# Optimization experiments

Hardware: AMD Instinct MI355X
Metric: run time of the kernel (lower is better)

Reference implementation:

```python
import jax, jax.numpy as jnp
import numpy as np

DIM = 1024
HEADS = 16
HEAD_DIM = 64
INNER = HEADS * HEAD_DIM  # 1024
SCALE = 8.0
LN_EPS = 1e-5
NORM_EPS = 1e-12  # F.normalize default eps


def layer_norm(x, g, b):
    m = jnp.mean(x, axis=-1, keepdims=True)
    v = jnp.mean((x - m) ** 2, axis=-1, keepdims=True)
    return (x - m) * jax.lax.rsqrt(v + LN_EPS) * g + b


def l2_normalize(x):
    n = jnp.sqrt(jnp.sum(x * x, axis=-1, keepdims=True))
    return x / jnp.maximum(n, NORM_EPS)


def setup_inputs() -> dict:
    key = jax.random.key(0)
    ks = jax.random.split(key, 8)
    B, N, T = 4, 4096, 256
    s = 0.02
    return {
        "x": jax.random.normal(ks[0], (B, N, DIM), jnp.float32),
        "context": jax.random.normal(ks[1], (B, T, DIM), jnp.float32),
        "Wq": jax.random.normal(ks[2], (DIM, INNER), jnp.float32) * s,
        "Wkv": jax.random.normal(ks[3], (DIM, 2 * INNER), jnp.float32) * s,
        "Wo": jax.random.normal(ks[4], (INNER, DIM), jnp.float32) * s,
        "null_kv": jax.random.normal(ks[5], (2, HEAD_DIM), jnp.float32),
        "q_scale": jnp.ones((HEAD_DIM,), jnp.float32),
        "k_scale": jnp.ones((HEAD_DIM,), jnp.float32),
        "ln_in_g": jnp.ones((DIM,), jnp.float32),
        "ln_in_b": jnp.zeros((DIM,), jnp.float32),
        "ln_ctx_g": jnp.ones((DIM,), jnp.float32),
        "ln_ctx_b": jnp.zeros((DIM,), jnp.float32),
        "ln_out_g": jnp.ones((DIM,), jnp.float32),
        "ln_out_b": jnp.zeros((DIM,), jnp.float32),
    }


def reference(x, context, Wq, Wkv, Wo, null_kv, q_scale, k_scale,
              ln_in_g, ln_in_b, ln_ctx_g, ln_ctx_b, ln_out_g, ln_out_b):
    B, N, _ = x.shape
    T = context.shape[1]
    xn = layer_norm(x, ln_in_g, ln_in_b)
    cn = layer_norm(context, ln_ctx_g, ln_ctx_b)
    q = xn @ Wq                      # [B, N, INNER]
    kv = cn @ Wkv                    # [B, T, 2*INNER]
    k, v = jnp.split(kv, 2, axis=-1)
    # split heads: b s (h d) -> b h s d
    def split_heads(t):
        b, s, _ = t.shape
        return t.reshape(b, s, HEADS, HEAD_DIM).transpose(0, 2, 1, 3)
    q, k, v = split_heads(q), split_heads(k), split_heads(v)
    # null kv token appended along kv-seq dim
    nk = jnp.broadcast_to(null_kv[0], (B, HEADS, 1, HEAD_DIM))
    nv = jnp.broadcast_to(null_kv[1], (B, HEADS, 1, HEAD_DIM))
    k = jnp.concatenate([k, nk], axis=2)   # [B, H, T+1, D]
    v = jnp.concatenate([v, nv], axis=2)
    q = l2_normalize(q) * q_scale
    k = l2_normalize(k) * k_scale
    scores = jnp.einsum('bhid,bhkd->bhik', q, k) * SCALE
    attn = jax.nn.softmax(scores, axis=-1)
    out = jnp.einsum('bhik,bhkd->bhid', attn, v)   # [B, H, N, D]
    out = out.transpose(0, 2, 1, 3).reshape(B, N, INNER)
    out = out @ Wo
    return layer_norm(out, ln_out_g, ln_out_b)
```

## Files before the change

### kernel.cpp

```cpp
#include <hip/hip_runtime.h>
#include <cstdint>
#include <cstddef>

typedef _Float16 f16;
typedef _Float16 f16x4 __attribute__((ext_vector_type(4)));
typedef _Float16 f16x8 __attribute__((ext_vector_type(8)));
typedef float f32x4 __attribute__((ext_vector_type(4)));

#define DIM 1024
#define B_ 4
#define N_ 4096
#define TKP 288
#define SCALE_ 8.0f
#define LOG2E 1.4426950408889634f

__device__ __forceinline__ void gload_lds16(const void* g, void* l) {
  __builtin_amdgcn_global_load_lds(
      reinterpret_cast<const __attribute__((address_space(1))) uint32_t*>(
          reinterpret_cast<uintptr_t>(g)),
      reinterpret_cast<__attribute__((address_space(3))) uint32_t*>(
          reinterpret_cast<uintptr_t>(l)),
      16, 0, 0);
}

__global__ void transpose_w_kernel(const float* __restrict__ W, f16* __restrict__ WT,
                                   int K, int N) {
  __shared__ float tile[32][33];
  int nt = N >> 5;
  int tk = blockIdx.x / nt, tn = blockIdx.x % nt;
  int tx = threadIdx.x & 31, ty = threadIdx.x >> 5;
#pragma unroll
  for (int p = 0; p < 32; p += 8)
    tile[ty + p][tx] = W[(size_t)(tk * 32 + ty + p) * N + tn * 32 + tx];
  __syncthreads();
#pragma unroll
  for (int p = 0; p < 32; p += 8)
    WT[(size_t)(tn * 32 + ty + p) * K + tk * 32 + tx] = (f16)tile[tx][ty + p];
}

template <typename OUT_T>
__global__ void ln_kernel(const float* __restrict__ in, const float* __restrict__ g,
                          const float* __restrict__ bb, OUT_T* __restrict__ out) {
  int row = blockIdx.x;
  int t = threadIdx.x;
  const float4* rp = (const float4*)(in + (size_t)row * DIM);
  float4 v = rp[t];
  float s = v.x + v.y + v.z + v.w;
  float ss = v.x * v.x + v.y * v.y + v.z * v.z + v.w * v.w;
#pragma unroll
  for (int m = 1; m < 64; m <<= 1) { s += __shfl_xor(s, m); ss += __shfl_xor(ss, m); }
  __shared__ float red[8];
  int w = t >> 6;
  if ((t & 63) == 0) { red[w * 2] = s; red[w * 2 + 1] = ss; }
  __syncthreads();
  s = red[0] + red[2] + red[4] + red[6];
  ss = red[1] + red[3] + red[5] + red[7];
  float mean = s * (1.0f / DIM);
  float var = ss * (1.0f / DIM) - mean * mean;
  float rstd = rsqrtf(var + 1e-5f);
  float4 gv = ((const float4*)g)[t];
  float4 bv = ((const float4*)bb)[t];
  float o0 = (v.x - mean) * rstd * gv.x + bv.x;
  float o1 = (v.y - mean) * rstd * gv.y + bv.y;
  float o2 = (v.z - mean) * rstd * gv.z + bv.z;
  float o3 = (v.w - mean) * rstd * gv.w + bv.w;
  if constexpr (sizeof(OUT_T) == 2) {
    f16x4 h = {(f16)o0, (f16)o1, (f16)o2, (f16)o3};
    *(f16x4*)((f16*)out + (size_t)row * DIM + t * 4) = h;
  } else {
    float4 o = {o0, o1, o2, o3};
    *(float4*)((float*)out + (size_t)row * DIM + t * 4) = o;
  }
}

template <bool OUT_F32>
__global__ __launch_bounds__(256, 2) void gemm_nt_kernel(
    const f16* __restrict__ A, const f16* __restrict__ Bt, void* __restrict__ C,
    int M, int N, int K) {
  __shared__ f16 As[128 * 64];
  __shared__ f16 Bs[128 * 64];
  int nb = N >> 7;
  int cpx = gridDim.x >> 3;
  int wg = ((int)blockIdx.x & 7) * cpx + ((int)blockIdx.x >> 3);
  int bm = wg / nb, bn = wg % nb;
  int t = threadIdx.x;
  int lane = t & 63, w = t >> 6;
  int wm = w >> 1, wn = w & 1;
  int r16 = lane & 15, g4 = lane >> 4;
  f32x4 acc[4][4] = {};
  for (int k0 = 0; k0 < K; k0 += 64) {
#pragma unroll
    for (int i = 0; i < 4; ++i) {
      int li = i * 256 + t;
      int r = li >> 3, c = li & 7;
      int kc = ((c ^ (r & 7)) << 3);
      gload_lds16(A + (size_t)(bm * 128 + r) * K + k0 + kc, (char*)As + li * 16);
      gload_lds16(Bt + (size_t)(bn * 128 + r) * K + k0 + kc, (char*)Bs + li * 16);
    }
    asm volatile("s_waitcnt vmcnt(0)" ::: "memory");
    __syncthreads();
#pragma unroll
    for (int ks = 0; ks < 2; ++ks) {
      f16x8 af[4], bf[4];
#pragma unroll
      for (int mi = 0; mi < 4; ++mi) {
        int r = wm * 64 + mi * 16 + r16;
        int cidx = ks * 4 + g4;
        af[mi] = *(const f16x8*)(As + r * 64 + ((cidx ^ (r & 7)) << 3));
      }
#pragma unroll
      for (int ni = 0; ni < 4; ++ni) {
        int r = wn * 64 + ni * 16 + r16;
        int cidx = ks * 4 + g4;
        bf[ni] = *(const f16x8*)(Bs + r * 64 + ((cidx ^ (r & 7)) << 3));
      }
#pragma unroll
      for (int mi = 0; mi < 4; ++mi)
#pragma unroll
        for (int ni = 0; ni < 4; ++ni)
          acc[mi][ni] = __builtin_amdgcn_mfma_f32_16x16x32_f16(af[mi], bf[ni],
                                                               acc[mi][ni], 0, 0, 0);
    }
    __syncthreads();
  }
  int cr0 = bm * 128 + wm * 64;
  int cc = bn * 128 + wn * 64 + r16;
#pragma unroll
  for (int mi = 0; mi < 4; ++mi)
#pragma unroll
    for (int ni = 0; ni < 4; ++ni)
#pragma unroll
      for (int j = 0; j < 4; ++j) {
        int row = cr0 + mi * 16 + g4 * 4 + j;
        int col = cc + ni * 16;
        if constexpr (OUT_F32)
          ((float*)C)[(size_t)row * N + col] = acc[mi][ni][j];
        else
          ((f16*)C)[(size_t)row * N + col] = (f16)acc[mi][ni][j];
      }
}

__global__ void prep_kv_kernel(const f16* __restrict__ kv, const float* __restrict__ nullkv,
                               const float* __restrict__ ks, f16* __restrict__ Karr,
                               f16* __restrict__ Varr) {
  int bh = blockIdx.x;
  int b = bh >> 4, h = bh & 15;
  int t = threadIdx.x;
  __shared__ f16 vt[256][65];
  const f16* krow = kv + (size_t)(b * 256 + t) * 2048 + h * 64;
  const f16* vrow = krow + 1024;
  f16x8 kd[8];
  float ss = 0.0f;
#pragma unroll
  for (int i = 0; i < 8; ++i) {
    kd[i] = *(const f16x8*)(krow + i * 8);
#pragma unroll
    for (int j = 0; j < 8; ++j) { float x = (float)kd[i][j]; ss += x * x; }
  }
  float inv = 1.0f / fmaxf(sqrtf(ss), 1e-12f);
  f16* kout = Karr + ((size_t)bh * TKP + t) * 64;
#pragma unroll
  for (int i = 0; i < 8; ++i) {
    f16x8 o;
#pragma unroll
    for (int j = 0; j < 8; ++j) o[j] = (f16)((float)kd[i][j] * inv * ks[i * 8 + j]);
    *(f16x8*)(kout + i * 8) = o;
  }
#pragma unroll
  for (int i = 0; i < 8; ++i) {
    f16x8 vv = *(const f16x8*)(vrow + i * 8);
#pragma unroll
    for (int j = 0; j < 8; ++j) vt[t][i * 8 + j] = vv[j];
  }
  if (t < 32) {
    f16* kr = Karr + ((size_t)bh * TKP + 256 + t) * 64;
    if (t == 0) {
      float ssn = 0.0f;
      for (int d = 0; d < 64; ++d) ssn += nullkv[d] * nullkv[d];
      float invn = 1.0f / fmaxf(sqrtf(ssn), 1e-12f);
      for (int d = 0; d < 64; ++d) kr[d] = (f16)(nullkv[d] * invn * ks[d]);
    } else {
      for (int d = 0; d < 64; ++d) kr[d] = (f16)0.0f;
    }
  }
  __syncthreads();
  f16* vbase = Varr + (size_t)bh * 64 * TKP;
  for (int d = 0; d < 64; ++d) vbase[(size_t)d * TKP + t] = vt[t][d];
#pragma unroll
  for (int i = 0; i < 8; ++i) {
    int idx = i * 256 + t;
    int d = idx >> 5, key = 256 + (idx & 31);
    vbase[(size_t)d * TKP + key] = (key == 256) ? (f16)nullkv[64 + d] : (f16)0.0f;
  }
}

__global__ __launch_bounds__(256, 2) void attn_kernel(
    const f16* __restrict__ Q, const f16* __restrict__ Karr,
    const f16* __restrict__ Varr, const float* __restrict__ qs,
    f16* __restrict__ O) {
  int qb = blockIdx.x & 15, bh = blockIdx.x >> 4;
  int b = bh >> 4, h = bh & 15;
  int t = threadIdx.x, lane = t & 63, w = t >> 6;
  int r16 = lane & 15, g4 = lane >> 4;
  int row0 = b * N_ + qb * 256 + w * 64;
  int col0 = h * 64;
  const f16* Kp = Karr + (size_t)bh * TKP * 64;
  const f16* Vp = Varr + (size_t)bh * 64 * TKP;
  __shared__ f16 Plds[4][64 * 40];
  f16* Pw = &Plds[w][0];
  float qsv[2][8];
#pragma unroll
  for (int kdh = 0; kdh < 2; ++kdh)
#pragma unroll
    for (int i = 0; i < 8; ++i) qsv[kdh][i] = qs[kdh * 32 + g4 * 8 + i];
  f16x8 qf[4][2];
#pragma unroll
  for (int mi = 0; mi < 4; ++mi) {
    float f[2][8];
    float ssq = 0.0f;
#pragma unroll
    for (int kdh = 0; kdh < 2; ++kdh) {
      f16x8 v = *(const f16x8*)(Q + (size_t)(row0 + mi * 16 + r16) * DIM +
                                col0 + kdh * 32 + g4 * 8);
#pragma unroll
      for (int i = 0; i < 8; ++i) { f[kdh][i] = (float)v[i]; ssq += f[kdh][i] * f[kdh][i]; }
    }
    ssq += __shfl_xor(ssq, 16);
    ssq += __shfl_xor(ssq, 32);
    float inv = 1.0f / fmaxf(sqrtf(ssq), 1e-12f);
#pragma unroll
    for (int kdh = 0; kdh < 2; ++kdh) {
      f16x8 o;
#pragma unroll
      for (int i = 0; i < 8; ++i) o[i] = (f16)(f[kdh][i] * inv * qsv[kdh][i]);
      qf[mi][kdh] = o;
    }
  }
  f32x4 o[4][4] = {};
  float mrow[4][4], lrow[4][4];
#pragma unroll
  for (int mi = 0; mi < 4; ++mi)
#pragma unroll
    for (int j = 0; j < 4; ++j) { mrow[mi][j] = -1e30f; lrow[mi][j] = 0.0f; }
  for (int kt = 0; kt < 9; ++kt) {
    int key0 = kt * 32;
    f16x8 kf[2][2];
#pragma unroll
    for (int ni = 0; ni < 2; ++ni)
#pragma unroll
      for (int kdh = 0; kdh < 2; ++kdh)
        kf[ni][kdh] = *(const f16x8*)(Kp + (size_t)(key0 + ni * 16 + r16) * 64 +
                                      kdh * 32 + g4 * 8);
    f32x4 s[4][2] = {};
#pragma unroll
    for (int kdh = 0; kdh < 2; ++kdh)
#pragma unroll
      for (int mi = 0; mi < 4; ++mi)
#pragma unroll
        for (int ni = 0; ni < 2; ++ni)
          s[mi][ni] = __builtin_amdgcn_mfma_f32_16x16x32_f16(qf[mi][kdh], kf[ni][kdh],
                                                             s[mi][ni], 0, 0, 0);
    bool va = (key0 + r16 <= 256), vb = (key0 + 16 + r16 <= 256);
#pragma unroll
    for (int mi = 0; mi < 4; ++mi) {
#pragma unroll
      for (int j = 0; j < 4; ++j) {
        float s0 = va ? s[mi][0][j] * SCALE_ : -1e30f;
        float s1 = vb ? s[mi][1][j] * SCALE_ : -1e30f;
        float tm = fmaxf(s0, s1);
        tm = fmaxf(tm, __shfl_xor(tm, 1));
        tm = fmaxf(tm, __shfl_xor(tm, 2));
        tm = fmaxf(tm, __shfl_xor(tm, 4));
        tm = fmaxf(tm, __shfl_xor(tm, 8));
        float nm = fmaxf(mrow[mi][j], tm);
        float corr = exp2f((mrow[mi][j] - nm) * LOG2E);
        mrow[mi][j] = nm;
        float p0 = exp2f((s0 - nm) * LOG2E);
        float p1 = exp2f((s1 - nm) * LOG2E);
        int prow = mi * 16 + g4 * 4 + j;
        Pw[prow * 40 + r16] = (f16)p0;
        Pw[prow * 40 + 16 + r16] = (f16)p1;
        float rs = p0 + p1;
        rs += __shfl_xor(rs, 1); rs += __shfl_xor(rs, 2);
        rs += __shfl_xor(rs, 4); rs += __shfl_xor(rs, 8);
        lrow[mi][j] = lrow[mi][j] * corr + rs;
#pragma unroll
        for (int nd = 0; nd < 4; ++nd) o[mi][nd][j] *= corr;
      }
    }
    f16x8 vf[4];
#pragma unroll
    for (int nd = 0; nd < 4; ++nd)
      vf[nd] = *(const f16x8*)(Vp + (size_t)(nd * 16 + r16) * TKP + key0 + g4 * 8);
#pragma unroll
    for (int mi = 0; mi < 4; ++mi) {
      f16x8 pa = *(const f16x8*)(Pw + (mi * 16 + r16) * 40 + g4 * 8);
#pragma unroll
      for (int nd = 0; nd < 4; ++nd)
        o[mi][nd] = __builtin_amdgcn_mfma_f32_16x16x32_f16(pa, vf[nd], o[mi][nd], 0, 0, 0);
    }
  }
#pragma unroll
  for (int mi = 0; mi < 4; ++mi)
#pragma unroll
    for (int j = 0; j < 4; ++j) {
      float inv = 1.0f / lrow[mi][j];
      int row = row0 + mi * 16 + g4 * 4 + j;
#pragma unroll
      for (int nd = 0; nd < 4; ++nd)
        O[(size_t)row * DIM + col0 + nd * 16 + r16] = (f16)(o[mi][nd][j] * inv);
    }
}

extern "C" void kernel_launch(void* const* d_in, const int* in_sizes, int n_in,
                              void* d_out, int out_size, void* d_ws, size_t ws_size,
                              hipStream_t stream) {
  const float* x      = (const float*)d_in[0];
  const float* ctx    = (const float*)d_in[1];
  const float* Wq     = (const float*)d_in[2];
  const float* Wkv    = (const float*)d_in[3];
  const float* Wo     = (const float*)d_in[4];
  const float* nullkv = (const float*)d_in[5];
  const float* qs     = (const float*)d_in[6];
  const float* ks     = (const float*)d_in[7];
  const float* g_in   = (const float*)d_in[8];
  const float* b_in   = (const float*)d_in[9];
  const float* g_ctx  = (const float*)d_in[10];
  const float* b_ctx  = (const float*)d_in[11];
  const float* g_out  = (const float*)d_in[12];
  const float* b_out  = (const float*)d_in[13];

  char* ws = (char*)d_ws;
  const size_t MB = 1ull << 20;
  f16* wqT   = (f16*)(ws + 0);
  f16* wkvT  = (f16*)(ws + 2 * MB);
  f16* woT   = (f16*)(ws + 6 * MB);
  f16* karr  = (f16*)(ws + 8 * MB);
  f16* varr  = (f16*)(ws + 11 * MB);
  f16* cn    = (f16*)(ws + 14 * MB);
  f16* kvb   = (f16*)(ws + 16 * MB);
  f16* xn    = (f16*)(ws + 20 * MB);
  f16* q_raw = (f16*)(ws + 52 * MB);
  f16* aout  = (f16*)(ws + 20 * MB);
  float* out2 = (float*)(ws + 52 * MB);

  transpose_w_kernel<<<1024, 256, 0, stream>>>(Wq, wqT, 1024, 1024);
  transpose_w_kernel<<<2048, 256, 0, stream>>>(Wkv, wkvT, 1024, 2048);
  transpose_w_kernel<<<1024, 256, 0, stream>>>(Wo, woT, 1024, 1024);

  ln_kernel<f16><<<16384, 256, 0, stream>>>(x, g_in, b_in, xn);
  ln_kernel<f16><<<1024, 256, 0, stream>>>(ctx, g_ctx, b_ctx, cn);

  gemm_nt_kernel<false><<<(16384 / 128) * (1024 / 128), 256, 0, stream>>>(
      xn, wqT, (void*)q_raw, 16384, 1024, 1024);
  gemm_nt_kernel<false><<<(1024 / 128) * (2048 / 128), 256, 0, stream>>>(
      cn, wkvT, (void*)kvb, 1024, 2048, 1024);

  prep_kv_kernel<<<64, 256, 0, stream>>>(kvb, nullkv, ks, karr, varr);

  attn_kernel<<<1024, 256, 0, stream>>>(q_raw, karr, varr, qs, aout);

  gemm_nt_kernel<true><<<(16384 / 128) * (1024 / 128), 256, 0, stream>>>(
      aout, woT, (void*)out2, 16384, 1024, 1024);

  ln_kernel<float><<<16384, 256, 0, stream>>>(out2, g_out, b_out, (float*)d_out);
}
```

Measured before the change: 404.2 us.

## Replace online softmax with fixed-bound exponent and halve attention tile per block

Because q and k are L2-normalized, scores are bounded by SCALE*max|q_scale|*max|k_scale|. The attention kernel therefore drops the running max, the rescaling and the per-tile shuffles, and uses that bound as a fixed softmax offset with one final row-sum reduction. It also halves rows per block (2048 blocks, occupancy hint 4), swizzles the block index, packs P stores with cvt_pkrtz, raises priority around the MFMA sections, and permutes V columns in prep so the packed P layout lines up. The fixed offset is exact in math but can underflow when the bound is loose, and the wider grid reloads K/V per block.

```diff
diff --git a/kernel.cpp b/kernel.cpp
--- a/kernel.cpp
+++ b/kernel.cpp
@@ -185,7 +185,8 @@
   }
   __syncthreads();
   f16* vbase = Varr + (size_t)bh * 64 * TKP;
-  for (int d = 0; d < 64; ++d) vbase[(size_t)d * TKP + t] = vt[t][d];
+  int pcol = (t & ~31) | (((t & 15) << 1) | ((t >> 4) & 1));
+  for (int d = 0; d < 64; ++d) vbase[(size_t)d * TKP + pcol] = vt[t][d];
 #pragma unroll
   for (int i = 0; i < 8; ++i) {
     int idx = i * 256 + t;
@@ -194,28 +195,37 @@
   }
 }
 
-__global__ __launch_bounds__(256, 2) void attn_kernel(
+__global__ __launch_bounds__(256, 4) void attn_kernel(
     const f16* __restrict__ Q, const f16* __restrict__ Karr,
     const f16* __restrict__ Varr, const float* __restrict__ qs,
-    f16* __restrict__ O) {
-  int qb = blockIdx.x & 15, bh = blockIdx.x >> 4;
+    const float* __restrict__ ksc, f16* __restrict__ O) {
+  int wgid = ((int)blockIdx.x & 7) * 256 + ((int)blockIdx.x >> 3);
+  int qb = wgid & 31, bh = wgid >> 5;
   int b = bh >> 4, h = bh & 15;
   int t = threadIdx.x, lane = t & 63, w = t >> 6;
   int r16 = lane & 15, g4 = lane >> 4;
-  int row0 = b * N_ + qb * 256 + w * 64;
+  int row0 = b * N_ + qb * 128 + w * 32;
   int col0 = h * 64;
   const f16* Kp = Karr + (size_t)bh * TKP * 64;
   const f16* Vp = Varr + (size_t)bh * 64 * TKP;
-  __shared__ f16 Plds[4][64 * 40];
+  __shared__ f16 Plds[4][32 * 40];
   f16* Pw = &Plds[w][0];
+  float mq = fabsf(qs[lane]), mk = fabsf(ksc[lane]);
+#pragma unroll
+  for (int m = 1; m < 64; m <<= 1) {
+    mq = fmaxf(mq, __shfl_xor(mq, m));
+    mk = fmaxf(mk, __shfl_xor(mk, m));
+  }
+  const float c1 = SCALE_ * LOG2E;
+  const float c2 = SCALE_ * mq * mk * LOG2E;
   float qsv[2][8];
 #pragma unroll
   for (int kdh = 0; kdh < 2; ++kdh)
 #pragma unroll
     for (int i = 0; i < 8; ++i) qsv[kdh][i] = qs[kdh * 32 + g4 * 8 + i];
-  f16x8 qf[4][2];
-#pragma unroll
-  for (int mi = 0; mi < 4; ++mi) {
+  f16x8 qf[2][2];
+#pragma unroll
+  for (int mi = 0; mi < 2; ++mi) {
     float f[2][8];
     float ssq = 0.0f;
 #pragma unroll
@@ -236,12 +246,8 @@
       qf[mi][kdh] = o;
     }
   }
-  f32x4 o[4][4] = {};
-  float mrow[4][4], lrow[4][4];
-#pragma unroll
-  for (int mi = 0; mi < 4; ++mi)
-#pragma unroll
-    for (int j = 0; j < 4; ++j) { mrow[mi][j] = -1e30f; lrow[mi][j] = 0.0f; }
+  f32x4 o[2][4] = {};
+  float part[2][4] = {};
   for (int kt = 0; kt < 9; ++kt) {
     int key0 = kt * 32;
     f16x8 kf[2][2];
@@ -251,60 +257,60 @@
       for (int kdh = 0; kdh < 2; ++kdh)
         kf[ni][kdh] = *(const f16x8*)(Kp + (size_t)(key0 + ni * 16 + r16) * 64 +
                                       kdh * 32 + g4 * 8);
-    f32x4 s[4][2] = {};
+    f32x4 s[2][2] = {};
+    __builtin_amdgcn_s_setprio(1);
 #pragma unroll
     for (int kdh = 0; kdh < 2; ++kdh)
 #pragma unroll
-      for (int mi = 0; mi < 4; ++mi)
+      for (int mi = 0; mi < 2; ++mi)
 #pragma unroll
         for (int ni = 0; ni < 2; ++ni)
           s[mi][ni] = __builtin_amdgcn_mfma_f32_16x16x32_f16(qf[mi][kdh], kf[ni][kdh],
                                                              s[mi][ni], 0, 0, 0);
+    __builtin_amdgcn_s_setprio(0);
     bool va = (key0 + r16 <= 256), vb = (key0 + 16 + r16 <= 256);
 #pragma unroll
-    for (int mi = 0; mi < 4; ++mi) {
+    for (int mi = 0; mi < 2; ++mi) {
 #pragma unroll
       for (int j = 0; j < 4; ++j) {
-        float s0 = va ? s[mi][0][j] * SCALE_ : -1e30f;
-        float s1 = vb ? s[mi][1][j] * SCALE_ : -1e30f;
-        float tm = fmaxf(s0, s1);
-        tm = fmaxf(tm, __shfl_xor(tm, 1));
-        tm = fmaxf(tm, __shfl_xor(tm, 2));
-        tm = fmaxf(tm, __shfl_xor(tm, 4));
-        tm = fmaxf(tm, __shfl_xor(tm, 8));
-        float nm = fmaxf(mrow[mi][j], tm);
-        float corr = exp2f((mrow[mi][j] - nm) * LOG2E);
-        mrow[mi][j] = nm;
-        float p0 = exp2f((s0 - nm) * LOG2E);
-        float p1 = exp2f((s1 - nm) * LOG2E);
+        float p0 = exp2f(s[mi][0][j] * c1 - c2);
+        float p1 = exp2f(s[mi][1][j] * c1 - c2);
+        p0 = va ? p0 : 0.0f;
+        p1 = vb ? p1 : 0.0f;
+        part[mi][j] += p0 + p1;
         int prow = mi * 16 + g4 * 4 + j;
-        Pw[prow * 40 + r16] = (f16)p0;
-        Pw[prow * 40 + 16 + r16] = (f16)p1;
-        float rs = p0 + p1;
-        rs += __shfl_xor(rs, 1); rs += __shfl_xor(rs, 2);
-        rs += __shfl_xor(rs, 4); rs += __shfl_xor(rs, 8);
-        lrow[mi][j] = lrow[mi][j] * corr + rs;
-#pragma unroll
-        for (int nd = 0; nd < 4; ++nd) o[mi][nd][j] *= corr;
+        auto pk = __builtin_amdgcn_cvt_pkrtz(p0, p1);
+        ((uint32_t*)(Pw + prow * 40))[r16] = __builtin_bit_cast(uint32_t, pk);
       }
     }
     f16x8 vf[4];
 #pragma unroll
     for (int nd = 0; nd < 4; ++nd)
       vf[nd] = *(const f16x8*)(Vp + (size_t)(nd * 16 + r16) * TKP + key0 + g4 * 8);
-#pragma unroll
-    for (int mi = 0; mi < 4; ++mi) {
+    __builtin_amdgcn_s_setprio(1);
+#pragma unroll
+    for (int mi = 0; mi < 2; ++mi) {
       f16x8 pa = *(const f16x8*)(Pw + (mi * 16 + r16) * 40 + g4 * 8);
 #pragma unroll
       for (int nd = 0; nd < 4; ++nd)
         o[mi][nd] = __builtin_amdgcn_mfma_f32_16x16x32_f16(pa, vf[nd], o[mi][nd], 0, 0, 0);
     }
-  }
-#pragma unroll
-  for (int mi = 0; mi < 4; ++mi)
+    __builtin_amdgcn_s_setprio(0);
+  }
+#pragma unroll
+  for (int mi = 0; mi < 2; ++mi)
 #pragma unroll
     for (int j = 0; j < 4; ++j) {
-      float inv = 1.0f / lrow[mi][j];
+      float v = part[mi][j];
+      v += __shfl_xor(v, 1); v += __shfl_xor(v, 2);
+      v += __shfl_xor(v, 4); v += __shfl_xor(v, 8);
+      part[mi][j] = v;
+    }
+#pragma unroll
+  for (int mi = 0; mi < 2; ++mi)
+#pragma unroll
+    for (int j = 0; j < 4; ++j) {
+      float inv = 1.0f / part[mi][j];
       int row = row0 + mi * 16 + g4 * 4 + j;
 #pragma unroll
       for (int nd = 0; nd < 4; ++nd)
@@ -358,7 +364,7 @@
 
   prep_kv_kernel<<<64, 256, 0, stream>>>(kvb, nullkv, ks, karr, varr);
 
-  attn_kernel<<<1024, 256, 0, stream>>>(q_raw, karr, varr, qs, aout);
+  attn_kernel<<<2048, 256, 0, stream>>>(q_raw, karr, varr, qs, ks, aout);
 
   gemm_nt_kernel<true><<<(16384 / 128) * (1024 / 128), 256, 0, stream>>>(
       aout, woT, (void*)out2, 16384, 1024, 1024);
```

After: 356.7 us. -11.7%, faster.
